# Kernel tuning notes

Measured on AMD Instinct MI355X. Metric: run time of the kernel, lower is better.

Reference implementation:

```python
import jax, jax.numpy as jnp
import numpy as np

N = 50000          # num nodes
E = 800000         # num directed edges
K = 10             # diffusion_iterations
ALPHA = 0.1        # teleportation_probability
D_IN, D_HID, N_CLS = 512, 128, 64


def _gcn_norm(edge_index, n):
    """Add self-loops and compute symmetric GCN normalization (PyG gcn_norm)."""
    loop = jnp.arange(n, dtype=edge_index.dtype)
    src = jnp.concatenate([edge_index[0], loop])  # message sources (x_j)
    dst = jnp.concatenate([edge_index[1], loop])  # aggregation targets
    deg = jax.ops.segment_sum(jnp.ones(src.shape[0], dtype=jnp.float32), dst,
                              num_segments=n)
    dinv = jnp.where(deg > 0, jax.lax.rsqrt(jnp.maximum(deg, 1.0)), 0.0)
    norm = dinv[src] * dinv[dst]  # [E+N]
    return src, dst, norm


def _appnp(x, src, dst, norm, n, k, alpha):
    """x_{t+1} = (1-alpha) * A_hat x_t + alpha * x_0, iterated k times."""
    h0 = x
    def step(xc, _):
        agg = jax.ops.segment_sum(xc[src] * norm[:, None], dst, num_segments=n)
        return (1.0 - alpha) * agg + alpha * h0, None
    xk, _ = jax.lax.scan(step, x, None, length=k)
    return xk


def setup_inputs() -> dict:
    key = jax.random.key(0)
    k1, k2, k3, k4 = jax.random.split(key, 4)
    x = jax.random.normal(k1, (N, D_IN), dtype=jnp.float32)
    edge_index = jax.random.randint(k2, (2, E), 0, N, dtype=jnp.int32)
    W1 = jax.random.normal(k3, (D_HID, D_IN), dtype=jnp.float32) / np.sqrt(D_IN)
    b1 = jnp.zeros((D_HID,), dtype=jnp.float32)
    W2 = jax.random.normal(k4, (N_CLS, D_HID), dtype=jnp.float32) / np.sqrt(D_HID)
    b2 = jnp.zeros((N_CLS,), dtype=jnp.float32)
    return {"x": x, "edge_index": edge_index, "W1": W1, "b1": b1,
            "W2": W2, "b2": b2}


def reference(x, edge_index, W1, b1, W2, b2):
    src, dst, norm = _gcn_norm(edge_index, N)
    # layer 0 (not last): linear + relu; since it is the second-to-last layer,
    # the recorded embedding is APPNP applied to its activation (x itself is
    # NOT replaced by the diffusion, matching the original forward).
    h1 = jax.nn.relu(x @ W1.T + b1)                    # [N, D_HID]
    emb1 = _appnp(h1, src, dst, norm, N, K, ALPHA)     # [N, D_HID]
    # last layer: linear only, then APPNP diffusion
    logits = h1 @ W2.T + b2                            # [N, N_CLS]
    out = _appnp(logits, src, dst, norm, N, K, ALPHA)  # [N, N_CLS]
    return (x, emb1, out)
```

## Files before the change

### kernel.cpp

```cpp
#include <hip/hip_runtime.h>

#define NN    50000
#define EE    800000
#define DIN   512
#define DH    128
#define NC    64
#define KITER 10
#define NSB   196

typedef __attribute__((ext_vector_type(8))) short short8;
typedef __attribute__((ext_vector_type(4))) short short4v;
typedef __attribute__((ext_vector_type(4))) float f32x4;

static __device__ __forceinline__ float bf2f(short u) {
  unsigned int x = ((unsigned int)(unsigned short)u) << 16;
  return __builtin_bit_cast(float, x);
}
static __device__ __forceinline__ short f2bf(float f) {
  unsigned int x = __builtin_bit_cast(unsigned int, f);
  unsigned int lsb = (x >> 16) & 1u;
  x += 0x7fffu + lsb;
  return (short)(x >> 16);
}

__global__ void k_copy4(const f32x4* __restrict__ src, f32x4* __restrict__ dst) {
  int i = blockIdx.x * 256 + threadIdx.x;
  dst[i] = src[i];
}

__global__ void k_f2bv(const float* __restrict__ src, short* __restrict__ dst) {
  int j = (blockIdx.x * 256 + threadIdx.x) * 4;
  f32x4 s = *(const f32x4*)(src + j);
  short4v o = { f2bf(s.x), f2bf(s.y), f2bf(s.z), f2bf(s.w) };
  *(short4v*)(dst + j) = o;
}

__global__ void k_count(const int* __restrict__ ei, int* __restrict__ cnt) {
  int e = blockIdx.x * 256 + threadIdx.x;
  if (e < EE) atomicAdd(&cnt[ei[EE + e]], 1);
}

__global__ void k_dinv(const int* __restrict__ cnt, float* __restrict__ dinv) {
  int i = blockIdx.x * 256 + threadIdx.x;
  if (i < NN) dinv[i] = rsqrtf((float)(cnt[i] + 1));
}

__global__ __launch_bounds__(256) void k_scan1(const int* __restrict__ cnt,
                                               int* __restrict__ rp,
                                               int* __restrict__ bsum) {
  __shared__ int wsum[4];
  int t = threadIdx.x, lane = t & 63, w = t >> 6;
  int i = blockIdx.x * 256 + t;
  int x = (i < NN) ? cnt[i] : 0;
  #pragma unroll
  for (int off = 1; off < 64; off <<= 1) {
    int y = __shfl_up(x, off);
    if (lane >= off) x += y;
  }
  if (lane == 63) wsum[w] = x;
  __syncthreads();
  int woff = 0;
  #pragma unroll
  for (int j = 0; j < 4; ++j) if (j < w) woff += wsum[j];
  x += woff;
  if (i < NN) rp[i + 1] = x;
  if (t == 255) bsum[blockIdx.x] = x;
}

__global__ __launch_bounds__(256) void k_scan2(int* __restrict__ bsum) {
  __shared__ int wsum[4];
  int t = threadIdx.x, lane = t & 63, w = t >> 6;
  int orig = (t < NSB) ? bsum[t] : 0;
  int x = orig;
  #pragma unroll
  for (int off = 1; off < 64; off <<= 1) {
    int y = __shfl_up(x, off);
    if (lane >= off) x += y;
  }
  if (lane == 63) wsum[w] = x;
  __syncthreads();
  int woff = 0;
  #pragma unroll
  for (int j = 0; j < 4; ++j) if (j < w) woff += wsum[j];
  x += woff;
  if (t < NSB) bsum[t] = x - orig;
}

__global__ __launch_bounds__(256) void k_scan3(int* __restrict__ rp,
                                               const int* __restrict__ bsum) {
  int i = blockIdx.x * 256 + threadIdx.x;
  if (i == 0) rp[0] = 0;
  if (i < NN) rp[i + 1] += bsum[blockIdx.x];
}

__global__ void k_fill(const int* __restrict__ ei, const int* __restrict__ rp,
                       int* __restrict__ fill, const float* __restrict__ dinv,
                       int* __restrict__ col, float* __restrict__ val) {
  int e = blockIdx.x * 256 + threadIdx.x;
  if (e < EE) {
    int s = ei[e], d = ei[EE + e];
    int pos = atomicAdd(&fill[d], 1);
    int idx = rp[d] + pos;
    col[idx] = s;
    val[idx] = dinv[s] * dinv[d];
  }
}

__global__ __launch_bounds__(256) void k_gemm1(const short* __restrict__ Xb,
                                               const short* __restrict__ W1b,
                                               const float* __restrict__ B1,
                                               short* __restrict__ h1,
                                               float* __restrict__ st0) {
  int w = threadIdx.x >> 6;
  int lane = threadIdx.x & 63;
  int q = lane >> 4, r = lane & 15;
  int m0 = blockIdx.x * 64 + w * 16;

  f32x4 acc[8];
  #pragma unroll
  for (int i = 0; i < 8; ++i) acc[i] = (f32x4){0.f, 0.f, 0.f, 0.f};

  int row_a = m0 + r;
  if (row_a >= NN) row_a = NN - 1;
  const short* xrow = Xb + (size_t)row_a * DIN + q * 8;

  for (int kc = 0; kc < DIN / 32; ++kc) {
    short8 a = *(const short8*)(xrow + kc * 32);
    #pragma unroll
    for (int nt = 0; nt < 8; ++nt) {
      const short* wrow = W1b + (size_t)(nt * 16 + r) * DIN + q * 8 + kc * 32;
      short8 b = *(const short8*)wrow;
      acc[nt] = __builtin_amdgcn_mfma_f32_16x16x32_bf16(a, b, acc[nt], 0, 0, 0);
    }
  }

  #pragma unroll
  for (int nt = 0; nt < 8; ++nt) {
    int n = nt * 16 + r;
    float bias = B1[n];
    #pragma unroll
    for (int reg = 0; reg < 4; ++reg) {
      int row = m0 + q * 4 + reg;
      if (row < NN) {
        float v = acc[nt][reg] + bias;
        v = v > 0.f ? v : 0.f;
        h1[(size_t)row * DH + n] = f2bf(v);
        st0[(size_t)row * DH + n] = v;
      }
    }
  }
}

__global__ __launch_bounds__(256) void k_step(const int* __restrict__ rp,
                                              const int* __restrict__ col,
                                              const float* __restrict__ val,
                                              const float* __restrict__ dinv,
                                              const float* __restrict__ xc,
                                              const short* __restrict__ h0,
                                              float* __restrict__ xn) {
  int g = blockIdx.x * 256 + threadIdx.x;
  int node = g >> 5, lane = g & 31;
  int beg = rp[node], end = rp[node + 1];
  const f32x4* xcv = (const f32x4*)xc;
  f32x4 acc = (f32x4){0.f, 0.f, 0.f, 0.f};
  for (int e = beg; e < end; ++e) {
    int s = col[e];
    float wgt = val[e];
    acc += xcv[(size_t)s * 32 + lane] * wgt;
  }
  float di = dinv[node];
  acc += xcv[(size_t)node * 32 + lane] * (di * di);
  short4v hv = ((const short4v*)h0)[node * 32 + lane];
  f32x4 h = { bf2f(hv.x), bf2f(hv.y), bf2f(hv.z), bf2f(hv.w) };
  ((f32x4*)xn)[(size_t)node * 32 + lane] = acc * 0.9f + h * 0.1f;
}

__global__ void k_vinit(float* __restrict__ v) {
  int i = blockIdx.x * 256 + threadIdx.x;
  if (i < NN) v[i] = 1.f;
}

__global__ void k_vstep(const int* __restrict__ rp, const int* __restrict__ col,
                        const float* __restrict__ val, const float* __restrict__ dinv,
                        const float* __restrict__ vc, float* __restrict__ vn) {
  int i = blockIdx.x * 256 + threadIdx.x;
  if (i >= NN) return;
  float s = 0.f;
  int end = rp[i + 1];
  for (int e = rp[i]; e < end; ++e) s += val[e] * vc[col[e]];
  float di = dinv[i];
  s += di * di * vc[i];
  vn[i] = 0.9f * s + 0.1f;
}

__global__ __launch_bounds__(256) void k_gemm2(const float* __restrict__ emb,
                                               const float* __restrict__ W2,
                                               const float* __restrict__ B2,
                                               const float* __restrict__ v,
                                               float* __restrict__ out2) {
  __shared__ float sW[NC][DH + 1];
  __shared__ float sb[NC];
  __shared__ float sE[32][DH + 1];
  int t = threadIdx.x;
  for (int i = t; i < NC * DH; i += 256) sW[i / DH][i % DH] = W2[i];
  if (t < NC) sb[t] = B2[t];
  int n0 = blockIdx.x * 32;
  for (int i = t; i < 32 * DH; i += 256) {
    int nl = i / DH, kk = i % DH;
    int node = n0 + nl;
    sE[nl][kk] = (node < NN) ? emb[(size_t)node * DH + kk] : 0.f;
  }
  __syncthreads();
  int nl = t >> 3, cb = t & 7;
  int node = n0 + nl;
  if (node >= NN) return;
  float vn = v[node];
  #pragma unroll
  for (int j = 0; j < 8; ++j) {
    int c = cb + 8 * j;
    float s = 0.f;
    #pragma unroll 4
    for (int k = 0; k < DH; ++k) s += sE[nl][k] * sW[c][k];
    s += vn * sb[c];
    out2[(size_t)node * NC + c] = s;
  }
}

extern "C" void kernel_launch(void* const* d_in, const int* in_sizes, int n_in,
                              void* d_out, int out_size, void* d_ws, size_t ws_size,
                              hipStream_t stream) {
  const float* X  = (const float*)d_in[0];
  const int*   EI = (const int*)d_in[1];
  const float* W1 = (const float*)d_in[2];
  const float* B1 = (const float*)d_in[3];
  const float* W2 = (const float*)d_in[4];
  const float* B2 = (const float*)d_in[5];

  float* out0 = (float*)d_out;
  float* out1 = (float*)d_out + 25600000;
  float* out2 = (float*)d_out + 32000000;

  char* xr = (char*)d_in[0];
  float* bufB = (float*)(xr);
  short* Xb   = (short*)(xr);
  float* bufA = (float*)(xr + 51200000);
  short* h1   = (short*)(xr + 76800000);
  int*   col  = (int*)  (xr + 89600000);
  float* val  = (float*)(xr + 92800000);
  int*   rp   = (int*)  (xr + 96000000);
  int*   cnt  = (int*)  (xr + 96200192);
  int*   fill = (int*)  (xr + 96400192);
  float* dinv = (float*)(xr + 96600192);
  float* va   = (float*)(xr + 96800192);
  float* vb   = (float*)(xr + 97000192);
  short* W1b  = (short*)(xr + 97200192);
  int*   bsum = (int*)  (xr + 97400192);

  k_copy4<<<dim3(25000), dim3(256), 0, stream>>>((const f32x4*)X, (f32x4*)out0);
  k_f2bv <<<dim3(25000), dim3(256), 0, stream>>>(out0, Xb);
  k_f2bv <<<dim3(64),    dim3(256), 0, stream>>>(W1, W1b);

  hipMemsetAsync(cnt, 0, 400000, stream);
  k_count<<<dim3(3125), dim3(256), 0, stream>>>(EI, cnt);
  k_dinv <<<dim3(196),  dim3(256), 0, stream>>>(cnt, dinv);
  k_scan1<<<dim3(NSB), dim3(256), 0, stream>>>(cnt, rp, bsum);
  k_scan2<<<dim3(1),   dim3(256), 0, stream>>>(bsum);
  k_scan3<<<dim3(NSB), dim3(256), 0, stream>>>(rp, bsum);
  k_fill <<<dim3(3125), dim3(256), 0, stream>>>(EI, rp, fill, dinv, col, val);

  k_gemm1<<<dim3(782),  dim3(256), 0, stream>>>(Xb, W1b, B1, h1, bufA);

  for (int it = 0; it < KITER; ++it) {
    const float* xc = (it & 1) ? bufB : bufA;
    float*       xn = (it & 1) ? bufA : bufB;
    k_step<<<dim3(6250), dim3(256), 0, stream>>>(rp, col, val, dinv, xc, h1, xn);
  }

  k_vinit<<<dim3(196), dim3(256), 0, stream>>>(va);
  for (int it = 0; it < KITER; ++it) {
    const float* vc = (it & 1) ? vb : va;
    float*       vn = (it & 1) ? va : vb;
    k_vstep<<<dim3(196), dim3(256), 0, stream>>>(rp, col, val, dinv, vc, vn);
  }

  k_gemm2<<<dim3(1563), dim3(256), 0, stream>>>(bufA, W2, B2, va, out2);
  k_copy4<<<dim3(6250), dim3(256), 0, stream>>>((const f32x4*)bufA, (f32x4*)out1);
}
```

Measured before the change: 1.269 ms.

## Fuse scalar diffusion into step kernel, write final iterate to output, merge copy and convert

Runs the per-node scalar v diffusion inside the feature diffusion kernel as extra blocks, so the separate vinit and vstep launches go away. The first iteration uses v=1 implicitly. The feature step now uses 64 lanes per node with float2 loads instead of 32 lanes with float4, and the last iterate is written straight into the output so the final copy is dropped. It also fuses the X copy with the bf16 conversion when a workspace is present, and folds dinv into scan1. This trims launches and memory passes, but the narrower loads may lower per-lane bandwidth efficiency.

Result: slower. 1.413 ms (+11.4%).

```diff
diff --git a/kernel.cpp b/kernel.cpp
--- a/kernel.cpp
+++ b/kernel.cpp
@@ -7,10 +7,12 @@
 #define NC    64
 #define KITER 10
 #define NSB   196
+#define XBLK  12500
 
 typedef __attribute__((ext_vector_type(8))) short short8;
 typedef __attribute__((ext_vector_type(4))) short short4v;
 typedef __attribute__((ext_vector_type(4))) float f32x4;
+typedef __attribute__((ext_vector_type(2))) float f32x2;
 
 static __device__ __forceinline__ float bf2f(short u) {
   unsigned int x = ((unsigned int)(unsigned short)u) << 16;
@@ -23,6 +25,15 @@
   return (short)(x >> 16);
 }
 
+__global__ void k_copy_conv(const f32x4* __restrict__ src, f32x4* __restrict__ dst,
+                            short4v* __restrict__ xb) {
+  int i = blockIdx.x * 256 + threadIdx.x;
+  f32x4 s = src[i];
+  dst[i] = s;
+  short4v o = { f2bf(s.x), f2bf(s.y), f2bf(s.z), f2bf(s.w) };
+  xb[i] = o;
+}
+
 __global__ void k_copy4(const f32x4* __restrict__ src, f32x4* __restrict__ dst) {
   int i = blockIdx.x * 256 + threadIdx.x;
   dst[i] = src[i];
@@ -40,18 +51,15 @@
   if (e < EE) atomicAdd(&cnt[ei[EE + e]], 1);
 }
 
-__global__ void k_dinv(const int* __restrict__ cnt, float* __restrict__ dinv) {
-  int i = blockIdx.x * 256 + threadIdx.x;
-  if (i < NN) dinv[i] = rsqrtf((float)(cnt[i] + 1));
-}
-
 __global__ __launch_bounds__(256) void k_scan1(const int* __restrict__ cnt,
                                                int* __restrict__ rp,
-                                               int* __restrict__ bsum) {
+                                               int* __restrict__ bsum,
+                                               float* __restrict__ dinv) {
   __shared__ int wsum[4];
   int t = threadIdx.x, lane = t & 63, w = t >> 6;
   int i = blockIdx.x * 256 + t;
   int x = (i < NN) ? cnt[i] : 0;
+  if (i < NN) dinv[i] = rsqrtf((float)(x + 1));
   #pragma unroll
   for (int off = 1; off < 64; off <<= 1) {
     int y = __shfl_up(x, off);
@@ -157,40 +165,42 @@
                                               const float* __restrict__ dinv,
                                               const float* __restrict__ xc,
                                               const short* __restrict__ h0,
-                                              float* __restrict__ xn) {
+                                              float* __restrict__ xn,
+                                              const float* __restrict__ vc,
+                                              float* __restrict__ vn,
+                                              int first) {
+  if (blockIdx.x >= XBLK) {
+    int i = (blockIdx.x - XBLK) * 256 + threadIdx.x;
+    if (i >= NN) return;
+    float s = 0.f;
+    int end = rp[i + 1];
+    if (first) {
+      for (int e = rp[i]; e < end; ++e) s += val[e];
+      float di = dinv[i];
+      s += di * di;
+    } else {
+      for (int e = rp[i]; e < end; ++e) s += val[e] * vc[col[e]];
+      float di = dinv[i];
+      s += di * di * vc[i];
+    }
+    vn[i] = 0.9f * s + 0.1f;
+    return;
+  }
   int g = blockIdx.x * 256 + threadIdx.x;
-  int node = g >> 5, lane = g & 31;
+  int node = g >> 6, lane = g & 63;
   int beg = rp[node], end = rp[node + 1];
-  const f32x4* xcv = (const f32x4*)xc;
-  f32x4 acc = (f32x4){0.f, 0.f, 0.f, 0.f};
+  const f32x2* xcv = (const f32x2*)xc;
+  f32x2 acc = (f32x2){0.f, 0.f};
   for (int e = beg; e < end; ++e) {
     int s = col[e];
     float wgt = val[e];
-    acc += xcv[(size_t)s * 32 + lane] * wgt;
+    acc += xcv[(size_t)s * 64 + lane] * wgt;
   }
   float di = dinv[node];
-  acc += xcv[(size_t)node * 32 + lane] * (di * di);
-  short4v hv = ((const short4v*)h0)[node * 32 + lane];
-  f32x4 h = { bf2f(hv.x), bf2f(hv.y), bf2f(hv.z), bf2f(hv.w) };
-  ((f32x4*)xn)[(size_t)node * 32 + lane] = acc * 0.9f + h * 0.1f;
-}
-
-__global__ void k_vinit(float* __restrict__ v) {
-  int i = blockIdx.x * 256 + threadIdx.x;
-  if (i < NN) v[i] = 1.f;
-}
-
-__global__ void k_vstep(const int* __restrict__ rp, const int* __restrict__ col,
-                        const float* __restrict__ val, const float* __restrict__ dinv,
-                        const float* __restrict__ vc, float* __restrict__ vn) {
-  int i = blockIdx.x * 256 + threadIdx.x;
-  if (i >= NN) return;
-  float s = 0.f;
-  int end = rp[i + 1];
-  for (int e = rp[i]; e < end; ++e) s += val[e] * vc[col[e]];
-  float di = dinv[i];
-  s += di * di * vc[i];
-  vn[i] = 0.9f * s + 0.1f;
+  acc += xcv[(size_t)node * 64 + lane] * (di * di);
+  unsigned int hv = ((const unsigned int*)h0)[(size_t)node * 64 + lane];
+  f32x2 h = { bf2f((short)(hv & 0xffffu)), bf2f((short)(hv >> 16)) };
+  ((f32x2*)xn)[(size_t)node * 64 + lane] = acc * 0.9f + h * 0.1f;
 }
 
 __global__ __launch_bounds__(256) void k_gemm2(const float* __restrict__ emb,
@@ -241,8 +251,11 @@
   float* out2 = (float*)d_out + 32000000;
 
   char* xr = (char*)d_in[0];
+  const size_t XB_BYTES = (size_t)NN * DIN * sizeof(short);
+  bool use_ws = (d_ws != nullptr) && (ws_size >= XB_BYTES);
+
   float* bufB = (float*)(xr);
-  short* Xb   = (short*)(xr);
+  short* Xb   = use_ws ? (short*)d_ws : (short*)(xr);
   float* bufA = (float*)(xr + 51200000);
   short* h1   = (short*)(xr + 76800000);
   int*   col  = (int*)  (xr + 89600000);
@@ -256,33 +269,32 @@
   short* W1b  = (short*)(xr + 97200192);
   int*   bsum = (int*)  (xr + 97400192);
 
-  k_copy4<<<dim3(25000), dim3(256), 0, stream>>>((const f32x4*)X, (f32x4*)out0);
-  k_f2bv <<<dim3(25000), dim3(256), 0, stream>>>(out0, Xb);
-  k_f2bv <<<dim3(64),    dim3(256), 0, stream>>>(W1, W1b);
+  if (use_ws) {
+    k_copy_conv<<<dim3(25000), dim3(256), 0, stream>>>(
+        (const f32x4*)X, (f32x4*)out0, (short4v*)Xb);
+  } else {
+    k_copy4<<<dim3(25000), dim3(256), 0, stream>>>((const f32x4*)X, (f32x4*)out0);
+    k_f2bv <<<dim3(25000), dim3(256), 0, stream>>>(out0, Xb);
+  }
+  k_f2bv <<<dim3(64), dim3(256), 0, stream>>>(W1, W1b);
 
   hipMemsetAsync(cnt, 0, 400000, stream);
   k_count<<<dim3(3125), dim3(256), 0, stream>>>(EI, cnt);
-  k_dinv <<<dim3(196),  dim3(256), 0, stream>>>(cnt, dinv);
-  k_scan1<<<dim3(NSB), dim3(256), 0, stream>>>(cnt, rp, bsum);
+  k_scan1<<<dim3(NSB), dim3(256), 0, stream>>>(cnt, rp, bsum, dinv);
   k_scan2<<<dim3(1),   dim3(256), 0, stream>>>(bsum);
   k_scan3<<<dim3(NSB), dim3(256), 0, stream>>>(rp, bsum);
   k_fill <<<dim3(3125), dim3(256), 0, stream>>>(EI, rp, fill, dinv, col, val);
 
-  k_gemm1<<<dim3(782),  dim3(256), 0, stream>>>(Xb, W1b, B1, h1, bufA);
+  k_gemm1<<<dim3(782), dim3(256), 0, stream>>>(Xb, W1b, B1, h1, bufA);
 
   for (int it = 0; it < KITER; ++it) {
     const float* xc = (it & 1) ? bufB : bufA;
-    float*       xn = (it & 1) ? bufA : bufB;
-    k_step<<<dim3(6250), dim3(256), 0, stream>>>(rp, col, val, dinv, xc, h1, xn);
-  }
-
-  k_vinit<<<dim3(196), dim3(256), 0, stream>>>(va);
-  for (int it = 0; it < KITER; ++it) {
-    const float* vc = (it & 1) ? vb : va;
-    float*       vn = (it & 1) ? va : vb;
-    k_vstep<<<dim3(196), dim3(256), 0, stream>>>(rp, col, val, dinv, vc, vn);
-  }
-
-  k_gemm2<<<dim3(1563), dim3(256), 0, stream>>>(bufA, W2, B2, va, out2);
-  k_copy4<<<dim3(6250), dim3(256), 0, stream>>>((const f32x4*)bufA, (f32x4*)out1);
-}
+    float*       xn = (it == KITER - 1) ? out1 : ((it & 1) ? bufA : bufB);
+    const float* vcp = (it & 1) ? vb : va;
+    float*       vnp = (it & 1) ? va : vb;
+    k_step<<<dim3(XBLK + NSB), dim3(256), 0, stream>>>(
+        rp, col, val, dinv, xc, h1, xn, vcp, vnp, it == 0 ? 1 : 0);
+  }
+
+  k_gemm2<<<dim3(1563), dim3(256), 0, stream>>>(out1, W2, B2, va, out2);
+}
```
